# Kernel tuning notes

Measured on AMD Instinct MI355X. Metric: run time of the kernel, lower is better.

## Reference

```python
import jax, jax.numpy as jnp
import numpy as np

H, C, G, DIM = 8, 16, 32, 3
G3 = G ** 3
EPS = 1e-5
# corner offsets of the trilinear cell: [8, 3]
_OFFS = jnp.array([[i, j, k] for i in (0, 1) for j in (0, 1) for k in (0, 1)], dtype=jnp.int32)


def _bn(x, gamma, beta, mean, var):
    # eval-mode BatchNorm1d: x [B, Ch, N], params [Ch]
    inv = jax.lax.rsqrt(var + EPS)
    return (x - mean[:, None]) * (inv * gamma)[:, None] + beta[:, None]


def _lattice_coords(lattice):
    # lattice: [B, H, 3, N] in (-1, 1) -> flat indices [B,H,8,N], trilinear weights [B,H,8,N]
    pos = (lattice + 1.0) * (0.5 * (G - 1))
    base = jnp.clip(jnp.floor(pos), 0.0, G - 2)
    frac = pos - base                                   # [B,H,3,N]
    base = base.astype(jnp.int32)
    corner = base[:, :, None, :, :] + _OFFS[None, None, :, :, None]   # [B,H,8,3,N]
    flat_idx = (corner[:, :, :, 0] * G + corner[:, :, :, 1]) * G + corner[:, :, :, 2]
    w = jnp.where(_OFFS[None, None, :, :, None] == 1,
                  frac[:, :, None, :, :], 1.0 - frac[:, :, None, :, :])  # [B,H,8,3,N]
    weights = jnp.prod(w, axis=3)                       # [B,H,8,N]
    return flat_idx, weights


def _splat(values, flat_idx, weights):
    # values [B,H,C,N] -> lattice [B,H,C,G3] via weighted scatter-add over 8 corners
    N = values.shape[-1]
    def one(v, idx, w):  # v [C,N], idx/w [8,N]
        contrib = (v[:, None, :] * w[None, :, :]).reshape(C, 8 * N)
        return jnp.zeros((C, G3), v.dtype).at[:, idx.reshape(-1)].add(contrib)
    return jax.vmap(jax.vmap(one))(values, flat_idx, weights)


def _slice(grid, flat_idx, weights):
    # grid [B,H,C,G3] -> per-point features [B,H,C,N] via weighted gather over 8 corners
    N = flat_idx.shape[-1]
    def one(g, idx, w):
        gathered = g[:, idx.reshape(-1)].reshape(C, 8, N)
        return jnp.sum(gathered * w[None, :, :], axis=1)
    return jax.vmap(jax.vmap(one))(grid, flat_idx, weights)


def setup_inputs() -> dict:
    key = jax.random.key(0)
    ks = jax.random.split(key, 20)
    B, D, N = 4, 64, 16384
    inp = {
        "x": jax.random.normal(ks[0], (B, D, N), jnp.float32),
        "orig_points": jax.random.normal(ks[1], (B, 3, N), jnp.float32),
        "w_kv": jax.random.normal(ks[2], (H * (C + 3), D), jnp.float32) * 0.1,
        "kbn_gamma": jax.random.normal(ks[3], (H * 3,), jnp.float32) * 0.1,
        "kbn_beta": jax.random.normal(ks[4], (H * 3,), jnp.float32) * 0.1,
        "kbn_mean": jax.random.normal(ks[5], (H * 3,), jnp.float32) * 0.1,
        "kbn_var": jax.random.uniform(ks[6], (H * 3,), jnp.float32, 0.5, 1.5),
        "vbn_gamma": jax.random.normal(ks[7], (H * C,), jnp.float32),
        "vbn_beta": jax.random.normal(ks[8], (H * C,), jnp.float32) * 0.1,
        "vbn_mean": jax.random.normal(ks[9], (H * C,), jnp.float32) * 0.1,
        "vbn_var": jax.random.uniform(ks[10], (H * C,), jnp.float32, 0.5, 1.5),
        "Wt": jnp.eye(3, dtype=jnp.float32)[None] + jax.random.normal(ks[11], (H, 3, 3), jnp.float32) * 0.05,
        "bt": jax.random.normal(ks[12], (H, 3), jnp.float32) * 0.1,
        "conv_w": jax.random.normal(ks[13], (H * C, C, 3, 3, 3), jnp.float32) * 0.05,
        "conv_b": jax.random.normal(ks[14], (H * C,), jnp.float32) * 0.05,
        "abn_gamma": jax.random.normal(ks[15], (H * C,), jnp.float32),
        "abn_beta": jax.random.normal(ks[16], (H * C,), jnp.float32) * 0.1,
        "abn_mean": jax.random.normal(ks[17], (H * C,), jnp.float32) * 0.1,
        "abn_var": jax.random.uniform(ks[18], (H * C,), jnp.float32, 0.5, 1.5),
    }
    return inp


def reference(x, orig_points, w_kv, kbn_gamma, kbn_beta, kbn_mean, kbn_var,
              vbn_gamma, vbn_beta, vbn_mean, vbn_var, Wt, bt, conv_w, conv_b,
              abn_gamma, abn_beta, abn_mean, abn_var):
    B, D, N = x.shape
    kv = jnp.einsum('od,bdn->bon', w_kv, x)                       # [B, H*(C+3), N]
    keys_off = _bn(kv[:, :H * 3], kbn_gamma, kbn_beta, kbn_mean, kbn_var)
    values = _bn(kv[:, H * 3:], vbn_gamma, vbn_beta, vbn_mean, vbn_var)
    keys_off = keys_off.reshape(B, H, 3, N)
    pts = orig_points[:, None, :, :] + keys_off                   # [B,H,3,N]
    tkeys = jnp.einsum('hij,bhjn->bhin', Wt, pts) + bt[None, :, :, None]
    lattice = jnp.tanh(tkeys)                                     # [B,H,3,N]
    flat_idx, weights = _lattice_coords(lattice)
    vals = values.reshape(B, H, C, N)
    grid = _splat(vals, flat_idx, weights).reshape(B, H * C, G, G, G)
    conv = jax.lax.conv_general_dilated(
        grid, conv_w, (1, 1, 1), 'SAME',
        dimension_numbers=('NCDHW', 'OIDHW', 'NCDHW'),
        feature_group_count=H) + conv_b[None, :, None, None, None]
    sliced = _slice(conv.reshape(B, H, C, G3), flat_idx, weights)  # [B,H,C,N]
    out = _bn(sliced.reshape(B, H * C, N), abn_gamma, abn_beta, abn_mean, abn_var)
    return jax.nn.relu(out)
```

## Files before the change

### kernel.cpp

```cpp
#include <hip/hip_runtime.h>
#include <hip/hip_bf16.h>

#define NB  4
#define NH  8
#define NC  16
#define ND  64
#define NN  16384
#define NG  32
#define NG3 32768
#define NKV 152
#define KEPS 1e-5f
#define TN  256

typedef __attribute__((ext_vector_type(8))) short bf16x8;
typedef __attribute__((ext_vector_type(4))) float f32x4;

__device__ __forceinline__ unsigned pack_bf2(float lo, float hi) {
    __hip_bfloat16 a = __float2bfloat16(lo);
    __hip_bfloat16 b = __float2bfloat16(hi);
    return (unsigned)(*(unsigned short*)&a) | ((unsigned)(*(unsigned short*)&b) << 16);
}
__device__ __forceinline__ float bf_lo(unsigned u) { return __uint_as_float(u << 16); }
__device__ __forceinline__ float bf_hi(unsigned u) { return __uint_as_float(u & 0xffff0000u); }

__global__ __launch_bounds__(256)
void k_front2(const float* __restrict__ x,
              const float* __restrict__ orig,
              const float* __restrict__ wkv,
              const float* __restrict__ kg, const float* __restrict__ kb,
              const float* __restrict__ km, const float* __restrict__ kvv,
              const float* __restrict__ vg, const float* __restrict__ vb,
              const float* __restrict__ vm, const float* __restrict__ vv,
              const float* __restrict__ Wt,
              const float* __restrict__ bt,
              unsigned short* __restrict__ valb,
              float4* __restrict__ pre,
              int* __restrict__ hist)
{
    __shared__ unsigned short xb[TN * 72];
    __shared__ float wk[24 * ND];
    __shared__ float ksc[24], ksh[24], vsc[128], vsh[128], wts[72], bts[24];
    const int tid = threadIdx.x;
    const int b  = blockIdx.x >> 6;
    const int n0 = (blockIdx.x & 63) * TN;
    const int n  = n0 + tid;

    for (int i = tid; i < 24 * ND; i += 256) wk[i] = wkv[i];
    if (tid < 24) {
        float s = rsqrtf(kvv[tid] + KEPS) * kg[tid];
        ksc[tid] = s;
        ksh[tid] = kb[tid] - km[tid] * s;
    }
    if (tid < 128) {
        float s = rsqrtf(vv[tid] + KEPS) * vg[tid];
        vsc[tid] = s;
        vsh[tid] = vb[tid] - vm[tid] * s;
    }
    if (tid < 72) wts[tid] = Wt[tid];
    if (tid < 24) bts[tid] = bt[tid];

    float xr[ND];
    #pragma unroll
    for (int d = 0; d < ND; ++d)
        xr[d] = x[((long)b * ND + d) * NN + n];
    #pragma unroll
    for (int j = 0; j < 8; ++j) {
        uint4 q;
        q.x = pack_bf2(xr[8*j+0], xr[8*j+1]);
        q.y = pack_bf2(xr[8*j+2], xr[8*j+3]);
        q.z = pack_bf2(xr[8*j+4], xr[8*j+5]);
        q.w = pack_bf2(xr[8*j+6], xr[8*j+7]);
        *(uint4*)(xb + tid * 72 + j * 8) = q;
    }
    __syncthreads();

    float ko[24];
    #pragma unroll 1
    for (int o = 0; o < 24; o += 4) {
        float s0 = 0.f, s1 = 0.f, s2 = 0.f, s3 = 0.f;
        #pragma unroll
        for (int dq = 0; dq < 16; ++dq) {
            const float4 w0 = *(const float4*)&wk[(o + 0) * ND + dq * 4];
            const float4 w1 = *(const float4*)&wk[(o + 1) * ND + dq * 4];
            const float4 w2 = *(const float4*)&wk[(o + 2) * ND + dq * 4];
            const float4 w3 = *(const float4*)&wk[(o + 3) * ND + dq * 4];
            float a0 = xr[4*dq], a1 = xr[4*dq+1], a2 = xr[4*dq+2], a3 = xr[4*dq+3];
            s0 = fmaf(w0.x, a0, fmaf(w0.y, a1, fmaf(w0.z, a2, fmaf(w0.w, a3, s0))));
            s1 = fmaf(w1.x, a0, fmaf(w1.y, a1, fmaf(w1.z, a2, fmaf(w1.w, a3, s1))));
            s2 = fmaf(w2.x, a0, fmaf(w2.y, a1, fmaf(w2.z, a2, fmaf(w2.w, a3, s2))));
            s3 = fmaf(w3.x, a0, fmaf(w3.y, a1, fmaf(w3.z, a2, fmaf(w3.w, a3, s3))));
        }
        ko[o + 0] = fmaf(s0, ksc[o + 0], ksh[o + 0]);
        ko[o + 1] = fmaf(s1, ksc[o + 1], ksh[o + 1]);
        ko[o + 2] = fmaf(s2, ksc[o + 2], ksh[o + 2]);
        ko[o + 3] = fmaf(s3, ksc[o + 3], ksh[o + 3]);
    }

    {
        const int lane = tid & 63;
        const int wv = tid >> 6;
        const int l15 = lane & 15, l4 = lane >> 4;

        bf16x8 bfr[2][2];
        float bsc[2], bsh[2];
        #pragma unroll
        for (int p = 0; p < 2; ++p) {
            int oc = (2 * wv + p) * 16 + l15;
            bsc[p] = vsc[oc];
            bsh[p] = vsh[oc];
            #pragma unroll
            for (int ks = 0; ks < 2; ++ks) {
                const float* wp = wkv + (24 + oc) * ND + ks * 32 + l4 * 8;
                float4 a = *(const float4*)wp;
                float4 c = *(const float4*)(wp + 4);
                uint4 q;
                q.x = pack_bf2(a.x, a.y); q.y = pack_bf2(a.z, a.w);
                q.z = pack_bf2(c.x, c.y); q.w = pack_bf2(c.z, c.w);
                bfr[p][ks] = *(bf16x8*)&q;
            }
        }

        #pragma unroll 1
        for (int nb = 0; nb < 16; ++nb) {
            bf16x8 a0 = *(const bf16x8*)(xb + (nb * 16 + l15) * 72 + l4 * 8);
            bf16x8 a1 = *(const bf16x8*)(xb + (nb * 16 + l15) * 72 + 32 + l4 * 8);
            #pragma unroll
            for (int p = 0; p < 2; ++p) {
                f32x4 acc = (f32x4){0.f, 0.f, 0.f, 0.f};
                acc = __builtin_amdgcn_mfma_f32_16x16x32_bf16(a0, bfr[p][0], acc, 0, 0, 0);
                acc = __builtin_amdgcn_mfma_f32_16x16x32_bf16(a1, bfr[p][1], acc, 0, 0, 0);
                int h = 2 * wv + p;
                unsigned short* vp = valb + (((long)(b * NH + h) * NN + n0 + nb * 16 + l4 * 4) * NC) + l15;
                #pragma unroll
                for (int r = 0; r < 4; ++r) {
                    __hip_bfloat16 hb = __float2bfloat16(fmaf(acc[r], bsc[p], bsh[p]));
                    vp[r * NC] = *(unsigned short*)&hb;
                }
            }
        }
    }

    const float o0 = orig[((long)b * 3 + 0) * NN + n];
    const float o1 = orig[((long)b * 3 + 1) * NN + n];
    const float o2 = orig[((long)b * 3 + 2) * NN + n];

    #pragma unroll 1
    for (int h = 0; h < NH; ++h) {
        float p0 = o0 + ko[h * 3 + 0];
        float p1 = o1 + ko[h * 3 + 1];
        float p2 = o2 + ko[h * 3 + 2];
        float t0 = fmaf(wts[h * 9 + 0], p0, fmaf(wts[h * 9 + 1], p1, fmaf(wts[h * 9 + 2], p2, bts[h * 3 + 0])));
        float t1 = fmaf(wts[h * 9 + 3], p0, fmaf(wts[h * 9 + 4], p1, fmaf(wts[h * 9 + 5], p2, bts[h * 3 + 1])));
        float t2 = fmaf(wts[h * 9 + 6], p0, fmaf(wts[h * 9 + 7], p1, fmaf(wts[h * 9 + 8], p2, bts[h * 3 + 2])));
        float l0 = tanhf(t0), l1 = tanhf(t1), l2 = tanhf(t2);
        float pos0 = (l0 + 1.f) * 15.5f;
        float pos1 = (l1 + 1.f) * 15.5f;
        float pos2 = (l2 + 1.f) * 15.5f;
        float b0 = fminf(fmaxf(floorf(pos0), 0.f), 30.f);
        float b1 = fminf(fmaxf(floorf(pos1), 0.f), 30.f);
        float b2 = fminf(fmaxf(floorf(pos2), 0.f), 30.f);
        int ix = (int)b0, iy = (int)b1, iz = (int)b2;
        float fx = pos0 - b0, fy = pos1 - b1, fz = pos2 - b2;
        int ibase = (ix * NG + iy) * NG + iz;
        float4 pr;
        pr.x = __int_as_float(ibase);
        pr.y = fx; pr.z = fy; pr.w = fz;
        int bh = b * NH + h;
        pre[(long)bh * NN + n] = pr;
        atomicAdd(&hist[bh * NG3 + ibase], 1);
    }
}

__global__ __launch_bounds__(1024)
void k_scan_cells(const int* __restrict__ hist, int* __restrict__ offs,
                  int* __restrict__ offs_live)
{
    __shared__ int tsum[1024];
    const int bh = blockIdx.x, tid = threadIdx.x;
    const int* hb = hist + (long)bh * NG3;

    int s = 0;
    #pragma unroll 4
    for (int j = 0; j < 32; ++j) s += hb[tid * 32 + j];
    tsum[tid] = s;
    __syncthreads();
    for (int d = 1; d < 1024; d <<= 1) {
        int t = (tid >= d) ? tsum[tid - d] : 0;
        __syncthreads();
        tsum[tid] += t;
        __syncthreads();
    }
    int run = bh * NN + tsum[tid] - s;
    int* ob = offs + (long)bh * NG3;
    int* lb = offs_live + (long)bh * NG3;
    #pragma unroll 4
    for (int j = 0; j < 32; ++j) {
        int c = tid * 32 + j;
        ob[c] = run;
        lb[c] = run;
        run += hb[c];
    }
}

__global__ __launch_bounds__(256)
void k_scatter2(const float4* __restrict__ pre, const unsigned short* __restrict__ valb,
                int* __restrict__ offs_live, uint4* __restrict__ rec)
{
    long t = (long)blockIdx.x * 256 + threadIdx.x;
    float4 r = pre[t];
    int ibase = __float_as_int(r.x);
    int bh = (int)(t >> 14);
    int slot = atomicAdd(&offs_live[(long)bh * NG3 + ibase], 1);
    const uint4* vp = (const uint4*)(valb + t * NC);
    uint4 v0 = vp[0], v1 = vp[1];
    uint4* out = rec + (long)slot * 3;
    out[0] = make_uint4(__float_as_uint(r.y), __float_as_uint(r.z), __float_as_uint(r.w), 0u);
    out[1] = v0;
    out[2] = v1;
}

__global__ __launch_bounds__(1024)
void k_splat6(const uint4* __restrict__ rec, const int* __restrict__ hist,
              const int* __restrict__ offs, unsigned short* __restrict__ gridb)
{
    __shared__ uint4 sr[1024 * 3];
    const int tid = threadIdx.x;
    const int rx = blockIdx.x & 31;
    const int bh = blockIdx.x >> 5;
    const int y = tid >> 5, z = tid & 31;
    const int zlo = (z > 0) ? z - 1 : 0;

    const int* hb = hist + (long)bh * NG3;
    const int* ob = offs + (long)bh * NG3;

    float acc[16];
    #pragma unroll
    for (int c = 0; c < 16; ++c) acc[c] = 0.f;

    #pragma unroll
    for (int dx = 0; dx < 2; ++dx) {
        int cx = rx - dx;
        if (cx < 0) continue;
        int st[2], sp[2], en[2];
        #pragma unroll
        for (int dy = 0; dy < 2; ++dy) {
            int cy = y - dy;
            bool valid = cy >= 0;
            int base = (cx << 10) | (cy << 5);
            int c1 = base | zlo;
            int c2 = base | z;
            st[dy] = valid ? ob[c1] : 0;
            sp[dy] = valid ? ob[c2] : 0;
            en[dy] = valid ? sp[dy] + hb[c2] : 0;
        }
        int pc0 = cx << 10;
        int ps = ob[pc0];
        int pe = ob[pc0 + 1023] + hb[pc0 + 1023];
        for (int cs = ps; cs < pe; cs += 1024) {
            int ce = min(cs + 1024, pe);
            __syncthreads();
            if (tid < ce - cs) {
                const uint4* R = rec + (long)(cs + tid) * 3;
                sr[tid * 3 + 0] = R[0];
                sr[tid * 3 + 1] = R[1];
                sr[tid * 3 + 2] = R[2];
            }
            __syncthreads();
            #pragma unroll
            for (int dy = 0; dy < 2; ++dy) {
                int ls = max(st[dy], cs);
                int le = min(en[dy], ce);
                int split = sp[dy];
                for (int r = ls; r < le; ++r) {
                    int k = (r - cs) * 3;
                    uint4 q0 = sr[k], q1 = sr[k + 1], q2 = sr[k + 2];
                    float fx = __uint_as_float(q0.x);
                    float fy = __uint_as_float(q0.y);
                    float fz = __uint_as_float(q0.z);
                    float wx = dx ? fx : 1.f - fx;
                    float wy = dy ? fy : 1.f - fy;
                    float wz = (r < split) ? fz : 1.f - fz;
                    float w = wx * wy * wz;
                    acc[0]  = fmaf(w, bf_lo(q1.x), acc[0]);
                    acc[1]  = fmaf(w, bf_hi(q1.x), acc[1]);
                    acc[2]  = fmaf(w, bf_lo(q1.y), acc[2]);
                    acc[3]  = fmaf(w, bf_hi(q1.y), acc[3]);
                    acc[4]  = fmaf(w, bf_lo(q1.z), acc[4]);
                    acc[5]  = fmaf(w, bf_hi(q1.z), acc[5]);
                    acc[6]  = fmaf(w, bf_lo(q1.w), acc[6]);
                    acc[7]  = fmaf(w, bf_hi(q1.w), acc[7]);
                    acc[8]  = fmaf(w, bf_lo(q2.x), acc[8]);
                    acc[9]  = fmaf(w, bf_hi(q2.x), acc[9]);
                    acc[10] = fmaf(w, bf_lo(q2.y), acc[10]);
                    acc[11] = fmaf(w, bf_hi(q2.y), acc[11]);
                    acc[12] = fmaf(w, bf_lo(q2.z), acc[12]);
                    acc[13] = fmaf(w, bf_hi(q2.z), acc[13]);
                    acc[14] = fmaf(w, bf_lo(q2.w), acc[14]);
                    acc[15] = fmaf(w, bf_hi(q2.w), acc[15]);
                }
            }
        }
    }

    uint4 q0, q1;
    q0.x = pack_bf2(acc[0],  acc[1]);  q0.y = pack_bf2(acc[2],  acc[3]);
    q0.z = pack_bf2(acc[4],  acc[5]);  q0.w = pack_bf2(acc[6],  acc[7]);
    q1.x = pack_bf2(acc[8],  acc[9]);  q1.y = pack_bf2(acc[10], acc[11]);
    q1.z = pack_bf2(acc[12], acc[13]); q1.w = pack_bf2(acc[14], acc[15]);
    uint4* gb = (uint4*)(gridb + ((long)bh * NG3 + (rx << 10) + tid) * NC);
    gb[0] = q0;
    gb[1] = q1;
}

__global__ __launch_bounds__(256)
void k_wprep(const float* __restrict__ cw, unsigned short* __restrict__ wpre)
{
    const int h = blockIdx.x;
    for (int e = threadIdx.x; e < 7168; e += 256) {
        int icl = e & 7, oc = (e >> 3) & 15, ihl = (e >> 7) & 1, tap = e >> 8;
        int ic = ihl * 8 + icl;
        float wv = (tap < 27) ? cw[(h * 16 + oc) * 432 + ic * 27 + tap] : 0.f;
        __hip_bfloat16 hbw = __float2bfloat16(wv);
        wpre[h * 7168 + e] = *(unsigned short*)&hbw;
    }
}

__global__ __launch_bounds__(512)
void k_conv5(const unsigned short* __restrict__ gridb,
             const unsigned short* __restrict__ wpre,
             const float* __restrict__ cb,
             unsigned short* __restrict__ convo)
{
    __shared__ unsigned short sg[2 * 6 * 10 * 34 * 8];
    __shared__ unsigned short sw[28 * 2 * 16 * 8];
    const int tid = threadIdx.x;
    const int bid = blockIdx.x;
    const int yt = bid & 3, xt = (bid >> 2) & 7, bh = bid >> 5;
    const int h = bh & 7;
    const int x0 = xt * 4, y0 = yt * 8;

    {
        const uint4* wsrc = (const uint4*)(wpre + (long)h * 7168);
        uint4* wdst = (uint4*)sw;
        for (int e = tid; e < 896; e += 512) wdst[e] = wsrc[e];
    }
    const unsigned short* gb = gridb + (long)bh * NG3 * 16;
    for (int e = tid; e < 2 * 6 * 10 * 34; e += 512) {
        int ihl = e & 1, c = e >> 1;
        int zz = c % 34, yu = c / 34;
        int yy = yu % 10, xx = yu / 10;
        int gx = x0 + xx - 1, gy = y0 + yy - 1, gz = zz - 1;
        uint4 v = make_uint4(0, 0, 0, 0);
        if ((unsigned)gx < NG && (unsigned)gy < NG && (unsigned)gz < NG)
            v = *(const uint4*)(gb + (((gx * NG + gy) * NG + gz) * 16 + ihl * 8));
        *(uint4*)(sg + ((((ihl * 6 + xx) * 10 + yy) * 34) + zz) * 8) = v;
    }
    __syncthreads();

    const int lane = tid & 63;
    const int w  = tid >> 6;
    const int wv = w & 3;
    const int zh = w >> 2;
    const int m  = lane & 15;
    const int l4 = lane >> 4;
    const int ihl = l4 & 1;
    const int tp = l4 >> 1;

    const int aLaneByte = ((((ihl * 6 + wv) * 10) * 34) + zh * 16 + m) * 16;
    const int bLaneByte = l4 * 256 + m * 16;
    const char* sgb = (const char*)sg;
    const char* swb = (const char*)sw;

    f32x4 acc[8];
    #pragma unroll
    for (int j = 0; j < 8; ++j) acc[j] = (f32x4){0.f, 0.f, 0.f, 0.f};

    #pragma unroll
    for (int p = 0; p < 14; ++p) {
        const int t0 = 2 * p, t1 = 2 * p + 1;
        const int ta0 = (t0 > 26) ? 26 : t0, ta1 = (t1 > 26) ? 26 : t1;
        const int off0 = ((ta0 / 9) * 340 + ((ta0 % 9) / 3) * 34 + (ta0 % 3)) * 16;
        const int off1 = ((ta1 / 9) * 340 + ((ta1 % 9) / 3) * 34 + (ta1 % 3)) * 16;
        const int aoff = aLaneByte + (tp ? off1 : off0);
        bf16x8 bfr = *(const bf16x8*)(swb + p * 1024 + bLaneByte);
        #pragma unroll
        for (int j = 0; j < 8; ++j) {
            bf16x8 afr = *(const bf16x8*)(sgb + aoff + j * 544);
            acc[j] = __builtin_amdgcn_mfma_f32_16x16x32_bf16(afr, bfr, acc[j], 0, 0, 0);
        }
    }

    const float bias = cb[h * 16 + m];
    unsigned short* cvb = convo + (long)bh * NG3 * NC;
    const int gx = x0 + wv;
    const int z0 = zh * 16;
    #pragma unroll
    for (int j = 0; j < 8; ++j) {
        int gy = y0 + j;
        long cellbase = (long)(gx * NG + gy) * NG + z0 + l4 * 4;
        #pragma unroll
        for (int r = 0; r < 4; ++r) {
            __hip_bfloat16 hb = __float2bfloat16(acc[j][r] + bias);
            cvb[(cellbase + r) * NC + m] = *(unsigned short*)&hb;
        }
    }
}

__global__ __launch_bounds__(256)
void k_slice(const unsigned short* __restrict__ convo, const float4* __restrict__ pre,
             const float* __restrict__ ag, const float* __restrict__ ab,
             const float* __restrict__ am, const float* __restrict__ av,
             float* __restrict__ out)
{
    __shared__ float asc[128], ash[128];
    const int tid = threadIdx.x;
    if (tid < 128) {
        float s = rsqrtf(av[tid] + KEPS) * ag[tid];
        asc[tid] = s;
        ash[tid] = ab[tid] - am[tid] * s;
    }
    __syncthreads();

    long t = (long)blockIdx.x * 256 + tid;
    long bh = t / NN;
    int n = (int)(t % NN);
    int b = (int)(bh >> 3), h = (int)(bh & 7);
    const unsigned short* g = convo + bh * (long)NG3 * NC;

    float4 r = pre[t];
    int ibase = __float_as_int(r.x);
    float fx = r.y, fy = r.z, fz = r.w;
    float gx = 1.f - fx, gy = 1.f - fy, gz = 1.f - fz;
    const float ws8[8] = {gx*gy*gz, gx*gy*fz, gx*fy*gz, gx*fy*fz,
                          fx*gy*gz, fx*gy*fz, fx*fy*gz, fx*fy*fz};
    const int offs8[8] = {0, 1, NG, NG + 1, NG*NG, NG*NG + 1, NG*NG + NG, NG*NG + NG + 1};

    float acc[NC];
    #pragma unroll
    for (int c = 0; c < NC; ++c) acc[c] = 0.f;
    #pragma unroll
    for (int ci = 0; ci < 8; ++ci) {
        float w = ws8[ci];
        const uint4* gc = (const uint4*)(g + (long)(ibase + offs8[ci]) * NC);
        uint4 u0 = gc[0], u1 = gc[1];
        acc[0]  = fmaf(w, bf_lo(u0.x), acc[0]);
        acc[1]  = fmaf(w, bf_hi(u0.x), acc[1]);
        acc[2]  = fmaf(w, bf_lo(u0.y), acc[2]);
        acc[3]  = fmaf(w, bf_hi(u0.y), acc[3]);
        acc[4]  = fmaf(w, bf_lo(u0.z), acc[4]);
        acc[5]  = fmaf(w, bf_hi(u0.z), acc[5]);
        acc[6]  = fmaf(w, bf_lo(u0.w), acc[6]);
        acc[7]  = fmaf(w, bf_hi(u0.w), acc[7]);
        acc[8]  = fmaf(w, bf_lo(u1.x), acc[8]);
        acc[9]  = fmaf(w, bf_hi(u1.x), acc[9]);
        acc[10] = fmaf(w, bf_lo(u1.y), acc[10]);
        acc[11] = fmaf(w, bf_hi(u1.y), acc[11]);
        acc[12] = fmaf(w, bf_lo(u1.z), acc[12]);
        acc[13] = fmaf(w, bf_hi(u1.z), acc[13]);
        acc[14] = fmaf(w, bf_lo(u1.w), acc[14]);
        acc[15] = fmaf(w, bf_hi(u1.w), acc[15]);
    }
    float* ob = out + ((long)b * 128 + h * 16) * NN + n;
    #pragma unroll
    for (int c = 0; c < NC; ++c) {
        float rr = fmaf(acc[c], asc[h * 16 + c], ash[h * 16 + c]);
        ob[(long)c * NN] = fmaxf(rr, 0.f);
    }
}

extern "C" void kernel_launch(void* const* d_in, const int* in_sizes, int n_in,
                              void* d_out, int out_size, void* d_ws, size_t ws_size,
                              hipStream_t stream)
{
    (void)in_sizes; (void)n_in; (void)out_size; (void)ws_size;
    const float* x    = (const float*)d_in[0];
    const float* orig = (const float*)d_in[1];
    const float* wkv  = (const float*)d_in[2];
    const float* kg   = (const float*)d_in[3];
    const float* kb   = (const float*)d_in[4];
    const float* km   = (const float*)d_in[5];
    const float* kvv  = (const float*)d_in[6];
    const float* vg   = (const float*)d_in[7];
    const float* vb   = (const float*)d_in[8];
    const float* vm   = (const float*)d_in[9];
    const float* vv   = (const float*)d_in[10];
    const float* Wt   = (const float*)d_in[11];
    const float* bt   = (const float*)d_in[12];
    const float* cw   = (const float*)d_in[13];
    const float* cb   = (const float*)d_in[14];
    const float* ag   = (const float*)d_in[15];
    const float* ab   = (const float*)d_in[16];
    const float* am   = (const float*)d_in[17];
    const float* av   = (const float*)d_in[18];

    char* ws = (char*)d_ws;
    float4*         pre       = (float4*)        (ws);
    int*            hist      = (int*)           (ws + 8388608);
    int*            offs      = (int*)           (ws + 12582912);
    int*            offs_live = (int*)           (ws + 16777216);
    unsigned short* valb      = (unsigned short*)(ws + 20971520);
    uint4*          rec       = (uint4*)         (ws + 37748736);
    unsigned short* gridb     = (unsigned short*)(ws + 62914560);
    unsigned short* wpre      = (unsigned short*)(ws + 96468992);
    unsigned short* convo     = (unsigned short*)(ws + 20971520);

    hipMemsetAsync(hist, 0, (size_t)NB * NH * NG3 * sizeof(int), stream);

    k_wprep<<<dim3(NH), dim3(256), 0, stream>>>(cw, wpre);

    k_front2<<<dim3(NB * 64), dim3(256), 0, stream>>>(
        x, orig, wkv, kg, kb, km, kvv, vg, vb, vm, vv, Wt, bt, valb, pre, hist);

    k_scan_cells<<<dim3(NB * NH), dim3(1024), 0, stream>>>(hist, offs, offs_live);

    k_scatter2<<<dim3((NB * NH * NN) / 256), dim3(256), 0, stream>>>(
        pre, valb, offs_live, rec);

    k_splat6<<<dim3(NB * NH * NG), dim3(1024), 0, stream>>>(rec, hist, offs, gridb);

    k_conv5<<<dim3(NB * NH * 32), dim3(512), 0, stream>>>(gridb, wpre, cb, convo);

    k_slice<<<dim3((NB * NH * NN) / 256), dim3(256), 0, stream>>>(
        convo, pre, ag, ab, am, av, (float*)d_out);
}
```

Measured before the change: 208.9 us.

## Split front kernel across head groups and zero histogram with custom kernel

The front kernel now launches twice as many blocks, each handling half of the heads (4 of 8) for a point tile. This cuts per-thread key-offset work and MFMA loops so more blocks can fill the GPU's compute units. In exchange the x tile is loaded and converted twice. The hipMemsetAsync on the histogram is replaced by a small custom zeroing kernel to lower launch/memset overhead.

```diff
diff --git a/kernel.cpp b/kernel.cpp
--- a/kernel.cpp
+++ b/kernel.cpp
@@ -24,7 +24,13 @@
 __device__ __forceinline__ float bf_hi(unsigned u) { return __uint_as_float(u & 0xffff0000u); }
 
 __global__ __launch_bounds__(256)
-void k_front2(const float* __restrict__ x,
+void k_zero(uint4* __restrict__ p)
+{
+    p[(long)blockIdx.x * 256 + threadIdx.x] = make_uint4(0, 0, 0, 0);
+}
+
+__global__ __launch_bounds__(256)
+void k_front3(const float* __restrict__ x,
               const float* __restrict__ orig,
               const float* __restrict__ wkv,
               const float* __restrict__ kg, const float* __restrict__ kb,
@@ -38,26 +44,30 @@
               int* __restrict__ hist)
 {
     __shared__ unsigned short xb[TN * 72];
-    __shared__ float wk[24 * ND];
-    __shared__ float ksc[24], ksh[24], vsc[128], vsh[128], wts[72], bts[24];
+    __shared__ float wk[12 * ND];
+    __shared__ float ksc[12], ksh[12], vsc[64], vsh[64], wts[36], bts[12];
     const int tid = threadIdx.x;
-    const int b  = blockIdx.x >> 6;
-    const int n0 = (blockIdx.x & 63) * TN;
+    const int hg   = blockIdx.x & 1;
+    const int tile = (blockIdx.x >> 1) & 63;
+    const int b    = blockIdx.x >> 7;
+    const int n0 = tile * TN;
     const int n  = n0 + tid;
 
-    for (int i = tid; i < 24 * ND; i += 256) wk[i] = wkv[i];
-    if (tid < 24) {
-        float s = rsqrtf(kvv[tid] + KEPS) * kg[tid];
+    for (int i = tid; i < 12 * ND; i += 256) wk[i] = wkv[hg * 768 + i];
+    if (tid < 12) {
+        int ch = hg * 12 + tid;
+        float s = rsqrtf(kvv[ch] + KEPS) * kg[ch];
         ksc[tid] = s;
-        ksh[tid] = kb[tid] - km[tid] * s;
-    }
-    if (tid < 128) {
-        float s = rsqrtf(vv[tid] + KEPS) * vg[tid];
+        ksh[tid] = kb[ch] - km[ch] * s;
+    }
+    if (tid < 64) {
+        int ch = hg * 64 + tid;
+        float s = rsqrtf(vv[ch] + KEPS) * vg[ch];
         vsc[tid] = s;
-        vsh[tid] = vb[tid] - vm[tid] * s;
-    }
-    if (tid < 72) wts[tid] = Wt[tid];
-    if (tid < 24) bts[tid] = bt[tid];
+        vsh[tid] = vb[ch] - vm[ch] * s;
+    }
+    if (tid < 36) wts[tid] = Wt[hg * 36 + tid];
+    if (tid < 12) bts[tid] = bt[hg * 12 + tid];
 
     float xr[ND];
     #pragma unroll
@@ -74,9 +84,9 @@
     }
     __syncthreads();
 
-    float ko[24];
+    float ko[12];
     #pragma unroll 1
-    for (int o = 0; o < 24; o += 4) {
+    for (int o = 0; o < 12; o += 4) {
         float s0 = 0.f, s1 = 0.f, s2 = 0.f, s3 = 0.f;
         #pragma unroll
         for (int dq = 0; dq < 16; ++dq) {
@@ -100,42 +110,35 @@
         const int lane = tid & 63;
         const int wv = tid >> 6;
         const int l15 = lane & 15, l4 = lane >> 4;
-
-        bf16x8 bfr[2][2];
-        float bsc[2], bsh[2];
+        const int h = hg * 4 + wv;
+        const int ocg = h * 16 + l15;
+        const float bsc = vsc[wv * 16 + l15];
+        const float bsh = vsh[wv * 16 + l15];
+
+        bf16x8 bfr[2];
         #pragma unroll
-        for (int p = 0; p < 2; ++p) {
-            int oc = (2 * wv + p) * 16 + l15;
-            bsc[p] = vsc[oc];
-            bsh[p] = vsh[oc];
-            #pragma unroll
-            for (int ks = 0; ks < 2; ++ks) {
-                const float* wp = wkv + (24 + oc) * ND + ks * 32 + l4 * 8;
-                float4 a = *(const float4*)wp;
-                float4 c = *(const float4*)(wp + 4);
-                uint4 q;
-                q.x = pack_bf2(a.x, a.y); q.y = pack_bf2(a.z, a.w);
-                q.z = pack_bf2(c.x, c.y); q.w = pack_bf2(c.z, c.w);
-                bfr[p][ks] = *(bf16x8*)&q;
-            }
+        for (int ks = 0; ks < 2; ++ks) {
+            const float* wp = wkv + (24 + ocg) * ND + ks * 32 + l4 * 8;
+            float4 a = *(const float4*)wp;
+            float4 c = *(const float4*)(wp + 4);
+            uint4 q;
+            q.x = pack_bf2(a.x, a.y); q.y = pack_bf2(a.z, a.w);
+            q.z = pack_bf2(c.x, c.y); q.w = pack_bf2(c.z, c.w);
+            bfr[ks] = *(bf16x8*)&q;
         }
 
         #pragma unroll 1
         for (int nb = 0; nb < 16; ++nb) {
             bf16x8 a0 = *(const bf16x8*)(xb + (nb * 16 + l15) * 72 + l4 * 8);
             bf16x8 a1 = *(const bf16x8*)(xb + (nb * 16 + l15) * 72 + 32 + l4 * 8);
+            f32x4 acc = (f32x4){0.f, 0.f, 0.f, 0.f};
+            acc = __builtin_amdgcn_mfma_f32_16x16x32_bf16(a0, bfr[0], acc, 0, 0, 0);
+            acc = __builtin_amdgcn_mfma_f32_16x16x32_bf16(a1, bfr[1], acc, 0, 0, 0);
+            unsigned short* vp = valb + (((long)(b * NH + h) * NN + n0 + nb * 16 + l4 * 4) * NC) + l15;
             #pragma unroll
-            for (int p = 0; p < 2; ++p) {
-                f32x4 acc = (f32x4){0.f, 0.f, 0.f, 0.f};
-                acc = __builtin_amdgcn_mfma_f32_16x16x32_bf16(a0, bfr[p][0], acc, 0, 0, 0);
-                acc = __builtin_amdgcn_mfma_f32_16x16x32_bf16(a1, bfr[p][1], acc, 0, 0, 0);
-                int h = 2 * wv + p;
-                unsigned short* vp = valb + (((long)(b * NH + h) * NN + n0 + nb * 16 + l4 * 4) * NC) + l15;
-                #pragma unroll
-                for (int r = 0; r < 4; ++r) {
-                    __hip_bfloat16 hb = __float2bfloat16(fmaf(acc[r], bsc[p], bsh[p]));
-                    vp[r * NC] = *(unsigned short*)&hb;
-                }
+            for (int r = 0; r < 4; ++r) {
+                __hip_bfloat16 hb = __float2bfloat16(fmaf(acc[r], bsc, bsh));
+                vp[r * NC] = *(unsigned short*)&hb;
             }
         }
     }
@@ -145,13 +148,13 @@
     const float o2 = orig[((long)b * 3 + 2) * NN + n];
 
     #pragma unroll 1
-    for (int h = 0; h < NH; ++h) {
-        float p0 = o0 + ko[h * 3 + 0];
-        float p1 = o1 + ko[h * 3 + 1];
-        float p2 = o2 + ko[h * 3 + 2];
-        float t0 = fmaf(wts[h * 9 + 0], p0, fmaf(wts[h * 9 + 1], p1, fmaf(wts[h * 9 + 2], p2, bts[h * 3 + 0])));
-        float t1 = fmaf(wts[h * 9 + 3], p0, fmaf(wts[h * 9 + 4], p1, fmaf(wts[h * 9 + 5], p2, bts[h * 3 + 1])));
-        float t2 = fmaf(wts[h * 9 + 6], p0, fmaf(wts[h * 9 + 7], p1, fmaf(wts[h * 9 + 8], p2, bts[h * 3 + 2])));
+    for (int lh = 0; lh < 4; ++lh) {
+        float p0 = o0 + ko[lh * 3 + 0];
+        float p1 = o1 + ko[lh * 3 + 1];
+        float p2 = o2 + ko[lh * 3 + 2];
+        float t0 = fmaf(wts[lh * 9 + 0], p0, fmaf(wts[lh * 9 + 1], p1, fmaf(wts[lh * 9 + 2], p2, bts[lh * 3 + 0])));
+        float t1 = fmaf(wts[lh * 9 + 3], p0, fmaf(wts[lh * 9 + 4], p1, fmaf(wts[lh * 9 + 5], p2, bts[lh * 3 + 1])));
+        float t2 = fmaf(wts[lh * 9 + 6], p0, fmaf(wts[lh * 9 + 7], p1, fmaf(wts[lh * 9 + 8], p2, bts[lh * 3 + 2])));
         float l0 = tanhf(t0), l1 = tanhf(t1), l2 = tanhf(t2);
         float pos0 = (l0 + 1.f) * 15.5f;
         float pos1 = (l1 + 1.f) * 15.5f;
@@ -165,7 +168,7 @@
         float4 pr;
         pr.x = __int_as_float(ibase);
         pr.y = fx; pr.z = fy; pr.w = fz;
-        int bh = b * NH + h;
+        int bh = b * NH + hg * 4 + lh;
         pre[(long)bh * NN + n] = pr;
         atomicAdd(&hist[bh * NG3 + ibase], 1);
     }
@@ -504,11 +507,11 @@
     unsigned short* wpre      = (unsigned short*)(ws + 96468992);
     unsigned short* convo     = (unsigned short*)(ws + 20971520);
 
-    hipMemsetAsync(hist, 0, (size_t)NB * NH * NG3 * sizeof(int), stream);
+    k_zero<<<dim3(1024), dim3(256), 0, stream>>>((uint4*)hist);
 
     k_wprep<<<dim3(NH), dim3(256), 0, stream>>>(cw, wpre);
 
-    k_front2<<<dim3(NB * 64), dim3(256), 0, stream>>>(
+    k_front3<<<dim3(NB * 128), dim3(256), 0, stream>>>(
         x, orig, wkv, kg, kb, km, kvv, vg, vb, vm, vv, Wt, bt, valb, pre, hist);
 
     k_scan_cells<<<dim3(NB * NH), dim3(1024), 0, stream>>>(hist, offs, offs_live);
```

Result: no change. 208.8 us (-0.1%).
